# Optimization experiments

Measured on AMD Instinct MI355X. Metric: run time of the kernel, lower is better.

Reference implementation:

```python
import jax, jax.numpy as jnp
import numpy as np

D, H, E, K, N, PROJ = 512, 1024, 8, 2, 65536, 256
C = N * K // E  # expert capacity (capacity_factor=1.0 over the full token count)
LOG100 = float(np.log(100.0))


def _l2norm(v, axis=-1):
    return v / (jnp.linalg.norm(v, axis=axis, keepdims=True) + 1e-12)


def _moe(x, mask, Wp, bp, sim, temp, W1, b1, W2, b2):
    # tutel 'cosine_top' gate: cosine sim between projected tokens and expert embeddings,
    # scaled by clamped learned temperature.
    logits = _l2norm(x @ Wp + bp) @ _l2norm(sim, axis=0)
    logits = logits * jnp.exp(jnp.minimum(temp, LOG100))
    gates_all = jax.nn.softmax(logits, axis=-1)
    g, idx = jax.lax.top_k(gates_all, K)                      # [N,K]
    g = g / (jnp.sum(g, axis=-1, keepdims=True) + 1e-9)       # normalize top-k gates
    g = g * mask[:, None]                                     # zero out tokens not in this domain
    e = idx.reshape(-1)                                       # [N*K] expert id per slot
    gflat = g.reshape(-1)
    valid = jnp.repeat(mask, K)                               # [N*K]
    oh = jax.nn.one_hot(e, E, dtype=jnp.float32) * valid[:, None]
    pos = (jnp.cumsum(oh, axis=0) * oh).sum(-1).astype(jnp.int32) - 1  # slot within expert
    keep = ((pos >= 0) & (pos < C)).astype(x.dtype)           # drop overflow / masked tokens
    posc = jnp.clip(pos, 0, C - 1)
    tok = jnp.arange(N * K, dtype=jnp.int32) // K
    # dispatch -> [E,C,D]
    xd = jnp.zeros((E, C, D), x.dtype).at[e, posc].add(x[tok] * keep[:, None])
    # grouped expert FFN
    h = jax.nn.relu(jnp.einsum('ecd,edh->ech', xd, W1) + b1[:, None, :])
    y = jnp.einsum('ech,ehd->ecd', h, W2) + b2[:, None, :]
    # combine back to tokens
    out = jnp.zeros((N, D), x.dtype).at[tok].add(y[e, posc] * (gflat * keep)[:, None])
    return out


def _make_params(key):
    ks = jax.random.split(key, 4)
    Wp = jax.random.normal(ks[0], (D, PROJ), jnp.float32) * 0.02
    bp = jnp.zeros((PROJ,), jnp.float32)
    sim = jax.random.normal(ks[1], (PROJ, E), jnp.float32) * 0.02
    temp = jnp.asarray(np.log(10.0), jnp.float32)
    W1 = jax.random.normal(ks[2], (E, D, H), jnp.float32) * (1.0 / np.sqrt(D))
    b1 = jnp.zeros((E, H), jnp.float32)
    W2 = jax.random.normal(ks[3], (E, H, D), jnp.float32) * (1.0 / np.sqrt(H))
    b2 = jnp.zeros((E, D), jnp.float32)
    return Wp, bp, sim, temp, W1, b1, W2, b2


def setup_inputs():
    key = jax.random.key(0)
    kx, kl, k1, k2, k3, ksc = jax.random.split(key, 6)
    inp = {
        'x': jax.random.normal(kx, (N, D), jnp.float32),
        'domain_label': jax.random.randint(kl, (N,), 0, 2),
        'domain_scale': jax.random.normal(ksc, (1,), jnp.float32) * 0.1,
    }
    for name, k in (('sh', k1), ('day', k2), ('nt', k3)):
        Wp, bp, sim, temp, W1, b1, W2, b2 = _make_params(k)
        inp.update({name + '_Wp': Wp, name + '_bp': bp, name + '_sim': sim, name + '_temp': temp,
                    name + '_W1': W1, name + '_b1': b1, name + '_W2': W2, name + '_b2': b2})
    return inp


def reference(x, domain_label, domain_scale,
              sh_Wp, sh_bp, sh_sim, sh_temp, sh_W1, sh_b1, sh_W2, sh_b2,
              day_Wp, day_bp, day_sim, day_temp, day_W1, day_b1, day_W2, day_b2,
              nt_Wp, nt_bp, nt_sim, nt_temp, nt_W1, nt_b1, nt_W2, nt_b2):
    ones = jnp.ones((N,), jnp.float32)
    day = (domain_label == 0).astype(jnp.float32)
    night = (domain_label == 1).astype(jnp.float32)
    f_shared = _moe(x, ones, sh_Wp, sh_bp, sh_sim, sh_temp, sh_W1, sh_b1, sh_W2, sh_b2)
    f_domain = (_moe(x, day, day_Wp, day_bp, day_sim, day_temp, day_W1, day_b1, day_W2, day_b2)
                + _moe(x, night, nt_Wp, nt_bp, nt_sim, nt_temp, nt_W1, nt_b1, nt_W2, nt_b2))
    return f_shared + domain_scale * f_domain
```

## Files before the change

kernel.cpp:

```cpp
#include <hip/hip_runtime.h>

#define NTOK 65536
#define DDIM 512
#define HDIM 1024
#define NEXP 8
#define PROJ 256
#define CAP  16384
#define NSLOT (2*NTOK)
#define LOG100 4.605170185988091f

typedef __attribute__((ext_vector_type(8))) short bf16x8;
typedef __attribute__((ext_vector_type(4))) short short4v;
typedef __attribute__((ext_vector_type(4))) float f32x4;

__device__ inline float bf2f(unsigned short u){
    union { float f; unsigned int i; } c; c.i = ((unsigned int)u) << 16; return c.f;
}
__device__ inline unsigned short f2bf(float f){
    union { float f; unsigned int i; } c; c.f = f;
    unsigned int x = c.i;
    return (unsigned short)((x + 0x7fffu + ((x >> 16) & 1u)) >> 16);
}
__device__ inline void gload16(const void* g, void* lds){
    __builtin_amdgcn_global_load_lds(
        (const __attribute__((address_space(1))) unsigned int*)g,
        (__attribute__((address_space(3))) unsigned int*)lds, 16, 0, 0);
}

__global__ void init_k(const float4* __restrict__ x, ushort4* __restrict__ xb,
                       float4* __restrict__ out){
    long i = (long)blockIdx.x * 256 + threadIdx.x;
    float4 f = x[i];
    ushort4 u; u.x = f2bf(f.x); u.y = f2bf(f.y); u.z = f2bf(f.z); u.w = f2bf(f.w);
    xb[i] = u;
    out[i] = float4{0.f, 0.f, 0.f, 0.f};
}

__device__ inline void trans_body(const float* in, unsigned short* out, int R, int C){
    int rbase = blockIdx.y * 32, cbase = blockIdx.x * 32;
    if (rbase >= R || cbase >= C) return;
    __shared__ float tile[32][33];
    int tx = threadIdx.x, ty = threadIdx.y;
    #pragma unroll
    for (int i = 0; i < 4; i++)
        tile[ty + i*8][tx] = in[(long)(rbase + ty + i*8) * C + cbase + tx];
    __syncthreads();
    #pragma unroll
    for (int i = 0; i < 4; i++)
        out[(long)(cbase + ty + i*8) * R + rbase + tx] = f2bf(tile[tx][ty + i*8]);
}

__global__ __launch_bounds__(256)
void trans2_k(const float* __restrict__ W1, const float* __restrict__ W2,
              unsigned short* __restrict__ W1T, unsigned short* __restrict__ W2T)
{
    int z = blockIdx.z;
    if (z < 8) trans_body(W1 + (size_t)z*DDIM*HDIM, W1T + (size_t)z*DDIM*HDIM, DDIM, HDIM);
    else       trans_body(W2 + (size_t)(z-8)*DDIM*HDIM, W2T + (size_t)(z-8)*DDIM*HDIM, HDIM, DDIM);
}

struct W12P { const float* W1[3]; const float* W2[3]; };
__global__ __launch_bounds__(256)
void transW12all_k(W12P wp, unsigned short* __restrict__ W1T3, unsigned short* __restrict__ W2T3)
{
    int z = blockIdx.z, m = z >> 4, piece = z & 15;
    if (piece < 8)
        trans_body(wp.W1[m] + (size_t)piece*DDIM*HDIM,
                   W1T3 + ((size_t)m*8 + piece)*DDIM*HDIM, DDIM, HDIM);
    else
        trans_body(wp.W2[m] + (size_t)(piece-8)*DDIM*HDIM,
                   W2T3 + ((size_t)m*8 + piece-8)*DDIM*HDIM, HDIM, DDIM);
}

struct TpArgs { const float* Wp[3]; };
__global__ __launch_bounds__(256)
void transWp_k(TpArgs ta, unsigned short* __restrict__ WpT3)
{
    int m = blockIdx.z;
    trans_body(ta.Wp[m], WpT3 + (size_t)m*PROJ*DDIM, DDIM, PROJ);
}

struct SimArgs { const float* sim[3]; };
__global__ void simn3_k(SimArgs sa, float* __restrict__ simn3){
    __shared__ float red[256];
    const float* sim = sa.sim[blockIdx.x];
    float* simn = simn3 + (size_t)blockIdx.x * PROJ * NEXP;
    int j = threadIdx.x;
    for (int e = 0; e < NEXP; e++){
        float v = sim[j*NEXP + e];
        red[j] = v*v;
        __syncthreads();
        for (int s = 128; s > 0; s >>= 1){
            if (j < s) red[j] += red[j + s];
            __syncthreads();
        }
        float nrm = sqrtf(red[0]) + 1e-12f;
        __syncthreads();
        simn[j*NEXP + e] = v / nrm;
    }
}

struct WprodArgs { const float* Wp[3]; const float* bp[3]; };
__global__ __launch_bounds__(256)
void wprod_k(WprodArgs wa, const float* __restrict__ simn3,
             float* __restrict__ Wn3, float* __restrict__ bd3)
{
    int m = blockIdx.x;
    __shared__ float Sn[PROJ*NEXP];
    const float* Wp = wa.Wp[m];
    int t = threadIdx.x;
    for (int i = t; i < PROJ*NEXP; i += 256) Sn[i] = simn3[(size_t)m*PROJ*NEXP + i];
    __syncthreads();
    for (int r = t; r < DDIM; r += 256){
        float d[8];
        #pragma unroll
        for (int e = 0; e < 8; e++) d[e] = 0.f;
        for (int p = 0; p < PROJ; p++){
            float w = Wp[(size_t)r*PROJ + p];
            #pragma unroll
            for (int e = 0; e < 8; e++) d[e] = fmaf(w, Sn[p*8+e], d[e]);
        }
        #pragma unroll
        for (int e = 0; e < 8; e++) Wn3[((size_t)m*DDIM + r)*8 + e] = d[e];
    }
    if (t < 8){
        float s = 0.f;
        for (int p = 0; p < PROJ; p++) s = fmaf(wa.bp[m][p], Sn[p*8+t], s);
        bd3[m*8 + t] = s;
    }
}

struct PssArgs { const float* bp[3]; };
__global__ __launch_bounds__(256)
void pss_k(const unsigned short* __restrict__ WpT3, const unsigned short* __restrict__ xb,
           PssArgs pa, float* __restrict__ ssbuf)
{
    __shared__ __align__(16) short As[128*32];
    __shared__ __align__(16) short Bs[128*32];
    __shared__ float ssl[2][128];
    const int m = blockIdx.z;
    const int row0 = blockIdx.x * 128;
    const int n0 = blockIdx.y * 128;
    const unsigned short* AT = WpT3 + (size_t)m * PROJ * DDIM;
    const float* bp = pa.bp[m];

    const int t = threadIdx.x, w = t >> 6, l = t & 63;
    const int qrow = l >> 2, kc = (l & 3) * 8;
    long arowg[2], browg[2];
    #pragma unroll
    for (int q = 0; q < 2; q++){
        arowg[q] = (long)(row0 + w*32 + q*16 + qrow) * DDIM;
        browg[q] = (long)(n0   + w*32 + q*16 + qrow) * DDIM;
    }
    const int wm = (w >> 1) * 64, wn = (w & 1) * 64;
    const int fr = l & 15, fk = l >> 4;
    const int koff = fk * 8, fk4 = fk * 4;

    f32x4 acc[4][4];
    #pragma unroll
    for (int i = 0; i < 4; i++)
        #pragma unroll
        for (int j = 0; j < 4; j++) acc[i][j] = (f32x4){0.f, 0.f, 0.f, 0.f};

    for (int k0 = 0; k0 < DDIM; k0 += 32){
        __syncthreads();
        #pragma unroll
        for (int q = 0; q < 2; q++) gload16(AT + arowg[q] + k0 + kc, As + w*1024 + q*512);
        #pragma unroll
        for (int q = 0; q < 2; q++) gload16(xb + browg[q] + k0 + kc, Bs + w*1024 + q*512);
        __syncthreads();
        bf16x8 af[4], bfv[4];
        #pragma unroll
        for (int i = 0; i < 4; i++) af[i]  = *(const bf16x8*)&As[(wm + i*16 + fr)*32 + koff];
        #pragma unroll
        for (int j = 0; j < 4; j++) bfv[j] = *(const bf16x8*)&Bs[(wn + j*16 + fr)*32 + koff];
        #pragma unroll
        for (int i = 0; i < 4; i++)
            #pragma unroll
            for (int j = 0; j < 4; j++)
                acc[i][j] = __builtin_amdgcn_mfma_f32_16x16x32_bf16(af[i], bfv[j], acc[i][j], 0, 0, 0);
    }

    float part[4];
    #pragma unroll
    for (int j = 0; j < 4; j++){
        float s = 0.f;
        #pragma unroll
        for (int i = 0; i < 4; i++){
            int mc = row0 + wm + i*16 + fk4;
            float4 bb = *(const float4*)(bp + mc);
            float v0 = acc[i][j][0] + bb.x;
            float v1 = acc[i][j][1] + bb.y;
            float v2 = acc[i][j][2] + bb.z;
            float v3 = acc[i][j][3] + bb.w;
            s += v0*v0 + v1*v1 + v2*v2 + v3*v3;
        }
        s += __shfl_xor(s, 16, 64);
        s += __shfl_xor(s, 32, 64);
        part[j] = s;
    }
    if (fk == 0){
        #pragma unroll
        for (int j = 0; j < 4; j++) ssl[w >> 1][wn + j*16 + fr] = part[j];
    }
    __syncthreads();
    if (t < 128)
        ssbuf[((size_t)blockIdx.x*3 + m)*NTOK + n0 + t] = ssl[0][t] + ssl[1][t];
}

struct GfArgs { const float* tp[3]; };
__global__ __launch_bounds__(256)
void gatefin3_k(const float* __restrict__ x, const int* __restrict__ label,
                const float* __restrict__ Wn3, const float* __restrict__ bd3,
                const float* __restrict__ ssbuf, GfArgs gf,
                int* __restrict__ idx3, float* __restrict__ gw3)
{
    __shared__ float pd[3][64][26];
    const int t = threadIdx.x;
    const int tok = t & 63;
    const int qu = __builtin_amdgcn_readfirstlane(t >> 6);
    const int n = blockIdx.x * 64 + tok;

    float dots[3][8];
    #pragma unroll
    for (int m = 0; m < 3; m++)
        #pragma unroll
        for (int e = 0; e < 8; e++) dots[m][e] = 0.f;

    const float4* xp = (const float4*)(x + (size_t)n * DDIM + qu * 128);
    for (int c = 0; c < 8; c++){
        float4 xv[4];
        #pragma unroll
        for (int u = 0; u < 4; u++) xv[u] = xp[c*4 + u];
        #pragma unroll
        for (int kk = 0; kk < 16; kk++){
            float a = (kk & 2) ? ((kk & 1) ? xv[kk>>2].w : xv[kk>>2].z)
                               : ((kk & 1) ? xv[kk>>2].y : xv[kk>>2].x);
            int k = qu*128 + c*16 + kk;
            #pragma unroll
            for (int m = 0; m < 3; m++){
                const float* wr = Wn3 + ((size_t)m*DDIM + k)*8;
                float4 w0 = *(const float4*)wr;
                float4 w1 = *(const float4*)(wr + 4);
                dots[m][0] = fmaf(a, w0.x, dots[m][0]);
                dots[m][1] = fmaf(a, w0.y, dots[m][1]);
                dots[m][2] = fmaf(a, w0.z, dots[m][2]);
                dots[m][3] = fmaf(a, w0.w, dots[m][3]);
                dots[m][4] = fmaf(a, w1.x, dots[m][4]);
                dots[m][5] = fmaf(a, w1.y, dots[m][5]);
                dots[m][6] = fmaf(a, w1.z, dots[m][6]);
                dots[m][7] = fmaf(a, w1.w, dots[m][7]);
            }
        }
    }
    if (qu != 0){
        #pragma unroll
        for (int m = 0; m < 3; m++)
            #pragma unroll
            for (int e = 0; e < 8; e++) pd[qu-1][tok][m*8+e] = dots[m][e];
    }
    __syncthreads();
    if (qu == 0){
        #pragma unroll
        for (int qq = 0; qq < 3; qq++)
            #pragma unroll
            for (int m = 0; m < 3; m++)
                #pragma unroll
                for (int e = 0; e < 8; e++) dots[m][e] += pd[qq][tok][m*8+e];

        int lab = label[n];
        #pragma unroll
        for (int m = 0; m < 3; m++){
            float ss = ssbuf[(0*3+m)*(size_t)NTOK + n] + ssbuf[(1*3+m)*(size_t)NTOK + n];
            float scale = expf(fminf(gf.tp[m][0], LOG100));
            float inv = scale / (sqrtf(ss) + 1e-12f);
            float l8[8], mx = -1e30f;
            #pragma unroll
            for (int e = 0; e < 8; e++){
                l8[e] = (dots[m][e] + bd3[m*8+e]) * inv;
                mx = fmaxf(mx, l8[e]);
            }
            float g[8], s = 0.f;
            #pragma unroll
            for (int e = 0; e < 8; e++){ g[e] = expf(l8[e] - mx); s += g[e]; }
            #pragma unroll
            for (int e = 0; e < 8; e++) g[e] /= s;
            int e0 = 0; float b0 = g[0];
            #pragma unroll
            for (int e = 1; e < 8; e++) if (g[e] > b0){ b0 = g[e]; e0 = e; }
            int e1 = (e0 == 0) ? 1 : 0; float b1v = g[e1];
            #pragma unroll
            for (int e = 0; e < 8; e++) if (e != e0 && g[e] > b1v){ b1v = g[e]; e1 = e; }
            float maskv = (m == 0) ? 1.f : ((lab == m - 1) ? 1.f : 0.f);
            float s2 = b0 + b1v + 1e-9f;
            size_t base = (size_t)m * NSLOT + 2*(size_t)n;
            gw3[base]   = b0 / s2 * maskv;
            gw3[base+1] = b1v / s2 * maskv;
            idx3[base]   = e0;
            idx3[base+1] = e1;
        }
    }
}

template<int BGATHER, int OMODE>
__device__ __forceinline__
void gemm_core_t(short* As, short* Bs,
                 const unsigned short* __restrict__ AT, const unsigned short* __restrict__ Bv,
                 const float* __restrict__ bias, void* __restrict__ Cout,
                 int Kd, int Mld, int row0, int col0, int limitN,
                 const int* __restrict__ rowidx, const int* __restrict__ otok,
                 const float* __restrict__ gs)
{
    const int t = threadIdx.x;
    const int w = t >> 6, l = t & 63;
    const int qrow = l >> 2;
    const int kc = (l & 3) * 8;

    long arowg[2], browg[2];
    #pragma unroll
    for (int q = 0; q < 2; q++){
        arowg[q] = (long)(row0 + w*32 + q*16 + qrow) * Kd;
        int s = col0 + w*32 + q*16 + qrow;
        int gi = s;
        if (BGATHER) gi = (s < limitN) ? rowidx[s] : 0;
        browg[q] = (long)gi * Kd;
    }

    const int wm = (w >> 1) * 64, wn = (w & 1) * 64;
    const int fr = l & 15, fk = l >> 4;
    const int koff = fk * 8, fk4 = fk * 4;

    f32x4 acc[4][4];
    #pragma unroll
    for (int i = 0; i < 4; i++)
        #pragma unroll
        for (int j = 0; j < 4; j++) acc[i][j] = (f32x4){0.f, 0.f, 0.f, 0.f};

    for (int k0 = 0; k0 < Kd; k0 += 32){
        __syncthreads();
        #pragma unroll
        for (int q = 0; q < 2; q++) gload16(AT + arowg[q] + k0 + kc, As + w*1024 + q*512);
        #pragma unroll
        for (int q = 0; q < 2; q++) gload16(Bv + browg[q] + k0 + kc, Bs + w*1024 + q*512);
        __syncthreads();
        bf16x8 af[4], bfv[4];
        #pragma unroll
        for (int i = 0; i < 4; i++) af[i]  = *(const bf16x8*)&As[(wm + i*16 + fr)*32 + koff];
        #pragma unroll
        for (int j = 0; j < 4; j++) bfv[j] = *(const bf16x8*)&Bs[(wn + j*16 + fr)*32 + koff];
        #pragma unroll
        for (int i = 0; i < 4; i++)
            #pragma unroll
            for (int j = 0; j < 4; j++)
                acc[i][j] = __builtin_amdgcn_mfma_f32_16x16x32_bf16(af[i], bfv[j], acc[i][j], 0, 0, 0);
    }

    #pragma unroll
    for (int i = 0; i < 4; i++){
        const int mc = row0 + wm + i*16 + fk4;
        float4 bb = *(const float4*)(bias + mc);
        #pragma unroll
        for (int j = 0; j < 4; j++){
            int s = col0 + wn + j*16 + fr;
            if (s < limitN){
                if (OMODE == 1){
                    ushort4 u;
                    u.x = f2bf(fmaxf(acc[i][j][0] + bb.x, 0.f));
                    u.y = f2bf(fmaxf(acc[i][j][1] + bb.y, 0.f));
                    u.z = f2bf(fmaxf(acc[i][j][2] + bb.z, 0.f));
                    u.w = f2bf(fmaxf(acc[i][j][3] + bb.w, 0.f));
                    *(ushort4*)((unsigned short*)Cout + (long)s * Mld + mc) = u;
                } else {
                    int tk = otok[s];
                    float g = gs[s];
                    float* op = (float*)Cout + (long)tk * Mld + mc;
                    float4 c = *(const float4*)op;
                    c.x += g * (acc[i][j][0] + bb.x);
                    c.y += g * (acc[i][j][1] + bb.y);
                    c.z += g * (acc[i][j][2] + bb.z);
                    c.w += g * (acc[i][j][3] + bb.w);
                    *(float4*)op = c;
                }
            }
        }
    }
}

template<int BGATHER, int OMODE>
__device__ __forceinline__
void gemm_core_t64(short* As, short* Bs,
                   const unsigned short* __restrict__ AT, const unsigned short* __restrict__ Bv,
                   const float* __restrict__ bias, void* __restrict__ Cout,
                   int Kd, int Mld, int row0, int col0, int limitN,
                   const int* __restrict__ rowidx, const int* __restrict__ otok,
                   const float* __restrict__ gs)
{
    const int t = threadIdx.x;
    const int w = t >> 6, l = t & 63;
    const int qrow = l >> 2;
    const int seg = (l & 3) * 8;

    long arowg[2], browg[2];
    #pragma unroll
    for (int q = 0; q < 2; q++){
        arowg[q] = (long)(row0 + w*32 + q*16 + qrow) * Kd;
        int s = col0 + w*32 + q*16 + qrow;
        int gi = s;
        if (BGATHER) gi = (s < limitN) ? rowidx[s] : 0;
        browg[q] = (long)gi * Kd;
    }

    const int wm = (w >> 1) * 64, wn = (w & 1) * 64;
    const int fr = l & 15, fk = l >> 4;
    const int koff = fk * 8, fk4 = fk * 4;

    f32x4 acc[4][4];
    #pragma unroll
    for (int i = 0; i < 4; i++)
        #pragma unroll
        for (int j = 0; j < 4; j++) acc[i][j] = (f32x4){0.f, 0.f, 0.f, 0.f};

    for (int k0 = 0; k0 < Kd; k0 += 64){
        __syncthreads();
        #pragma unroll
        for (int ks = 0; ks < 2; ks++)
            #pragma unroll
            for (int q = 0; q < 2; q++)
                gload16(AT + arowg[q] + k0 + ks*32 + seg, As + ks*4096 + w*1024 + q*512);
        #pragma unroll
        for (int ks = 0; ks < 2; ks++)
            #pragma unroll
            for (int q = 0; q < 2; q++)
                gload16(Bv + browg[q] + k0 + ks*32 + seg, Bs + ks*4096 + w*1024 + q*512);
        __syncthreads();
        #pragma unroll
        for (int ks = 0; ks < 2; ks++){
            bf16x8 af[4], bfv[4];
            #pragma unroll
            for (int i = 0; i < 4; i++) af[i]  = *(const bf16x8*)&As[ks*4096 + (wm + i*16 + fr)*32 + koff];
            #pragma unroll
            for (int j = 0; j < 4; j++) bfv[j] = *(const bf16x8*)&Bs[ks*4096 + (wn + j*16 + fr)*32 + koff];
            #pragma unroll
            for (int i = 0; i < 4; i++)
                #pragma unroll
                for (int j = 0; j < 4; j++)
                    acc[i][j] = __builtin_amdgcn_mfma_f32_16x16x32_bf16(af[i], bfv[j], acc[i][j], 0, 0, 0);
        }
    }

    #pragma unroll
    for (int i = 0; i < 4; i++){
        const int mc = row0 + wm + i*16 + fk4;
        float4 bb = *(const float4*)(bias + mc);
        #pragma unroll
        for (int j = 0; j < 4; j++){
            int s = col0 + wn + j*16 + fr;
            if (s < limitN){
                if (OMODE == 1){
                    ushort4 u;
                    u.x = f2bf(fmaxf(acc[i][j][0] + bb.x, 0.f));
                    u.y = f2bf(fmaxf(acc[i][j][1] + bb.y, 0.f));
                    u.z = f2bf(fmaxf(acc[i][j][2] + bb.z, 0.f));
                    u.w = f2bf(fmaxf(acc[i][j][3] + bb.w, 0.f));
                    *(ushort4*)((unsigned short*)Cout + (long)s * Mld + mc) = u;
                } else {
                    int tk = otok[s];
                    float g = gs[s];
                    float* op = (float*)Cout + (long)tk * Mld + mc;
                    float4 c = *(const float4*)op;
                    c.x += g * (acc[i][j][0] + bb.x);
                    c.y += g * (acc[i][j][1] + bb.y);
                    c.z += g * (acc[i][j][2] + bb.z);
                    c.w += g * (acc[i][j][3] + bb.w);
                    *(float4*)op = c;
                }
            }
        }
    }
}

__device__ __forceinline__
void gemm_core_y64(short* lds,
                   const unsigned short* __restrict__ AT, const unsigned short* __restrict__ Bv,
                   const float* __restrict__ bias, float* __restrict__ out,
                   int row0, int col0, int limitN,
                   const int* __restrict__ otok, const float* __restrict__ gs)
{
    short* As = lds;
    short* Bs = lds + 4096;
    const int t = threadIdx.x, w = t >> 6, l = t & 63;
    const int seg = (l & 3) * 8;

    const long arow = (long)(row0 + w*16 + (l >> 2)) * HDIM;
    long brow[2];
    #pragma unroll
    for (int hh = 0; hh < 2; hh++)
        brow[hh] = (long)(col0 + w*32 + hh*16 + (l >> 2)) * HDIM;

    const int wm = (w >> 1) * 32, wn = (w & 1) * 64;
    const int fr = l & 15, fk = l >> 4;
    const int koff = fk * 8, fk4 = fk * 4;

    f32x4 acc[2][4];
    #pragma unroll
    for (int i = 0; i < 2; i++)
        #pragma unroll
        for (int j = 0; j < 4; j++) acc[i][j] = (f32x4){0.f, 0.f, 0.f, 0.f};

    for (int k0 = 0; k0 < HDIM; k0 += 64){
        __syncthreads();
        #pragma unroll
        for (int ks = 0; ks < 2; ks++)
            gload16(AT + arow + k0 + ks*32 + seg, As + ks*2048 + w*512);
        #pragma unroll
        for (int ks = 0; ks < 2; ks++)
            #pragma unroll
            for (int hh = 0; hh < 2; hh++)
                gload16(Bv + brow[hh] + k0 + ks*32 + seg, Bs + ks*4096 + w*1024 + hh*512);
        __syncthreads();
        #pragma unroll
        for (int ks = 0; ks < 2; ks++){
            bf16x8 af[2], bfv[4];
            #pragma unroll
            for (int i = 0; i < 2; i++)
                af[i] = *(const bf16x8*)&As[ks*2048 + (wm + i*16 + fr)*32 + koff];
            #pragma unroll
            for (int j = 0; j < 4; j++)
                bfv[j] = *(const bf16x8*)&Bs[ks*4096 + (wn + j*16 + fr)*32 + koff];
            #pragma unroll
            for (int i = 0; i < 2; i++)
                #pragma unroll
                for (int j = 0; j < 4; j++)
                    acc[i][j] = __builtin_amdgcn_mfma_f32_16x16x32_bf16(af[i], bfv[j], acc[i][j], 0, 0, 0);
        }
    }

    #pragma unroll
    for (int i = 0; i < 2; i++){
        const int mc = row0 + wm + i*16 + fk4;
        float4 bb = *(const float4*)(bias + mc);
        #pragma unroll
        for (int j = 0; j < 4; j++){
            int s = col0 + wn + j*16 + fr;
            if (s < limitN){
                int tk = otok[s];
                float g = gs[s];
                float* op = out + (long)tk * DDIM + mc;
                float4 c = *(const float4*)op;
                c.x += g * (acc[i][j][0] + bb.x);
                c.y += g * (acc[i][j][1] + bb.y);
                c.z += g * (acc[i][j][2] + bb.z);
                c.w += g * (acc[i][j][3] + bb.w);
                *(float4*)op = c;
            }
        }
    }
}

template<int BGATHER, int OMODE>
__global__ __launch_bounds__(256)
void mgemm3_k(const unsigned short* __restrict__ AT, const unsigned short* __restrict__ Bv,
              const float* __restrict__ bias, void* __restrict__ Cout,
              int Kd, int Mld,
              const int* __restrict__ rowidx, const int* __restrict__ otok,
              const float* __restrict__ gs, const int* __restrict__ cntp, int cnti)
{
    __shared__ __align__(16) short As[128*32];
    __shared__ __align__(16) short Bs[128*32];
    int limit = cntp[cnti]; if (limit > CAP) limit = CAP;
    int row0 = blockIdx.x * 128, col0 = blockIdx.y * 128;
    if (col0 >= limit) return;
    gemm_core_t<BGATHER, OMODE>(As, Bs, AT, Bv, bias, Cout, Kd, Mld,
                                row0, col0, limit, rowidx, otok, gs);
}

struct FfnP { const float* b1[3]; const float* b2[3]; };
__global__ __launch_bounds__(256)
void ffnA_k(const unsigned short* __restrict__ xb,
            const unsigned short* __restrict__ W1T3, const unsigned short* __restrict__ W2T3,
            FfnP fp, unsigned short* __restrict__ h0, unsigned short* __restrict__ h1,
            float* __restrict__ out,
            const int* __restrict__ tok3, const float* __restrict__ gslot3,
            const int* __restrict__ cntk3, int ge)
{
    __shared__ __align__(16) short lds[16384];
    const int bx = blockIdx.x, by = blockIdx.y;
    const int col0 = bx * 128;
    if (by < 8){
        if (ge >= 24) return;
        int m = ge >> 3, e = ge & 7;
        int limit = cntk3[m*16 + e]; if (limit > CAP) limit = CAP;
        if (col0 >= limit) return;
        unsigned short* hd = (ge & 1) ? h1 : h0;
        gemm_core_t64<1, 1>(lds, lds + 8192,
                            W1T3 + ((size_t)(m*8+e))*HDIM*DDIM, xb, fp.b1[m] + (size_t)e*HDIM,
                            hd, DDIM, HDIM, by*128, col0, limit,
                            tok3 + ((size_t)m*NEXP + e)*CAP, nullptr, nullptr);
    } else {
        int gy = ge - 1; if (gy < 0) return;
        int m = gy >> 3, e = gy & 7;
        int limit = cntk3[m*16 + e]; if (limit > CAP) limit = CAP;
        if (col0 >= limit) return;
        const unsigned short* hs = (gy & 1) ? h1 : h0;
        gemm_core_t64<0, 3>(lds, lds + 8192,
                            W2T3 + ((size_t)(m*8+e))*DDIM*HDIM, hs, fp.b2[m] + (size_t)e*DDIM,
                            out, HDIM, DDIM, (by-8)*128, col0, limit,
                            nullptr, tok3 + ((size_t)m*NEXP + e)*CAP,
                            gslot3 + ((size_t)m*NEXP + e)*CAP);
    }
}

__global__ __launch_bounds__(256)
void ffnB_k(const unsigned short* __restrict__ xb,
            const unsigned short* __restrict__ W1T, const float* __restrict__ b1,
            const unsigned short* __restrict__ W2T, const float* __restrict__ b2,
            unsigned short* __restrict__ h0, unsigned short* __restrict__ h1,
            float* __restrict__ out,
            const int* __restrict__ tok, const float* __restrict__ gslot,
            const int* __restrict__ cntk, int eh)
{
    __shared__ __align__(16) short lds[12288];
    const int bx = blockIdx.x, by = blockIdx.y;
    const int col0 = bx * 128;
    if (by < 8){
        if (eh > 7) return;
        int limit = cntk[eh]; if (limit > CAP) limit = CAP;
        if (col0 >= limit) return;
        unsigned short* hd = (eh & 1) ? h1 : h0;
        gemm_core_t<1, 1>(lds, lds + 4096,
                          W1T + (size_t)eh*HDIM*DDIM, xb, b1 + (size_t)eh*HDIM,
                          hd, DDIM, HDIM, by*128, col0, limit,
                          tok + (size_t)eh*CAP, nullptr, nullptr);
    } else {
        int ey = eh - 1; if (ey < 0) return;
        int limit = cntk[ey]; if (limit > CAP) limit = CAP;
        if (col0 >= limit) return;
        const unsigned short* hs = (ey & 1) ? h1 : h0;
        gemm_core_y64(lds, W2T + (size_t)ey*DDIM*HDIM, hs, b2 + (size_t)ey*DDIM,
                      out, (by-8)*64, col0, limit,
                      tok + (size_t)ey*CAP, gslot + (size_t)ey*CAP);
    }
}

__global__ __launch_bounds__(1024)
void rank_count3_k(const int* __restrict__ idx3, const int* __restrict__ label,
                   int* __restrict__ bcnt3)
{
    __shared__ int c[NEXP];
    const int m = blockIdx.y;
    const int* idx = idx3 + (size_t)m * NSLOT;
    int t = threadIdx.x;
    if (t < NEXP) c[t] = 0;
    __syncthreads();
    int s = blockIdx.x * 1024 + t;
    int n = s >> 1;
    int e = idx[s];
    bool valid = (m == 0) || (label[n] == m - 1);
    if (valid) atomicAdd(&c[e], 1);
    __syncthreads();
    if (t < NEXP) bcnt3[((size_t)m*128 + blockIdx.x)*NEXP + t] = c[t];
}

__global__ void rank_scan3_k(const int* __restrict__ bcnt3, int* __restrict__ boff3,
                             int* __restrict__ cntk3)
{
    int m = blockIdx.x, e = threadIdx.x;
    if (e < NEXP){
        int run = 0;
        for (int b = 0; b < NSLOT/1024; b++){
            boff3[((size_t)m*128 + b)*NEXP + e] = run;
            run += bcnt3[((size_t)m*128 + b)*NEXP + e];
        }
        cntk3[m*16 + e] = run < CAP ? run : CAP;
    }
}

__global__ __launch_bounds__(1024)
void rank_assign3_k(const int* __restrict__ idx3, const int* __restrict__ label,
                    const int* __restrict__ boff3, const float* __restrict__ gw3,
                    const float* __restrict__ dscale,
                    int* __restrict__ tok3, float* __restrict__ gs3)
{
    __shared__ int wcnt[16][NEXP];
    __shared__ int woff[16][NEXP];
    const int m = blockIdx.y;
    const int* idx = idx3 + (size_t)m * NSLOT;
    const float* gw = gw3 + (size_t)m * NSLOT;
    int t = threadIdx.x;
    int s = blockIdx.x * 1024 + t;
    int n = s >> 1;
    int e = idx[s];
    bool valid = (m == 0) || (label[n] == m - 1);
    int w = t >> 6, lane = t & 63;
    unsigned long long lt = (lane == 0) ? 0ull : ((1ull << lane) - 1ull);
    int myrank = 0;
    #pragma unroll
    for (int ei = 0; ei < NEXP; ei++){
        unsigned long long bal = __ballot(valid && (e == ei));
        if (ei == e) myrank = __popcll(bal & lt);
        if (lane == 0) wcnt[w][ei] = __popcll(bal);
    }
    __syncthreads();
    if (t < NEXP){
        int run = boff3[((size_t)m*128 + blockIdx.x)*NEXP + t];
        for (int w2 = 0; w2 < 16; w2++){
            woff[w2][t] = run;
            run += wcnt[w2][t];
        }
    }
    __syncthreads();
    int pos = woff[w][e] + myrank;
    bool keep = valid && (pos < CAP);
    if (keep){
        float scale = (m > 0) ? dscale[0] : 1.f;
        tok3[((size_t)m*NEXP + e)*CAP + pos] = n;
        gs3[((size_t)m*NEXP + e)*CAP + pos] = gw[s] * scale;
    }
}

extern "C" void kernel_launch(void* const* d_in, const int* in_sizes, int n_in,
                              void* d_out, int out_size, void* d_ws, size_t ws_size,
                              hipStream_t stream)
{
    (void)in_sizes; (void)n_in; (void)out_size;
    const float* x      = (const float*)d_in[0];
    const int*   label  = (const int*)  d_in[1];
    const float* dscale = (const float*)d_in[2];
    float* out = (float*)d_out;

    const size_t XB  = (size_t)NTOK * DDIM * 2;
    const size_t HS  = (size_t)CAP * HDIM * 2;
    const size_t WPT = (size_t)3 * PROJ * DDIM * 2;
    const size_t SS  = (size_t)2 * 3 * NTOK * 4;
    const size_t WN  = (size_t)3 * DDIM * 8 * 4;
    const size_t SMALL = WPT + SS + WN + 256 +
                         (size_t)3*PROJ*NEXP*4 +
                         (size_t)3*NSLOT*4*2 +
                         (size_t)3*NEXP*CAP*4*2 +
                         (size_t)3*128*NEXP*4*2 + 256;
    const size_t W12A = (size_t)2 * 3 * NEXP * DDIM * HDIM * 2;
    const size_t W12B = (size_t)2 * NEXP * DDIM * HDIM * 2;
    const size_t common = XB + HS + SMALL;

    int tier;
    if      (ws_size >= common + HS + W12A) tier = 0;
    else if (ws_size >= common + HS + W12B) tier = 1;
    else if (ws_size >= common + W12B)      tier = 2;
    else return;

    char* p = (char*)d_ws;
    unsigned short* xb   = (unsigned short*)p; p += XB;
    unsigned short* h0   = (unsigned short*)p; p += HS;
    unsigned short* WpT3 = (unsigned short*)p; p += WPT;
    float* ssbuf = (float*)p;  p += SS;
    float* Wn3   = (float*)p;  p += WN;
    float* bd3   = (float*)p;  p += 256;
    float* simn3 = (float*)p;  p += (size_t)3*PROJ*NEXP*4;
    int*   idx3  = (int*)p;    p += (size_t)3*NSLOT*4;
    float* gw3   = (float*)p;  p += (size_t)3*NSLOT*4;
    int*   tok3  = (int*)p;    p += (size_t)3*NEXP*CAP*4;
    float* gslot3= (float*)p;  p += (size_t)3*NEXP*CAP*4;
    int*   bcnt3 = (int*)p;    p += (size_t)3*128*NEXP*4;
    int*   boff3 = (int*)p;    p += (size_t)3*128*NEXP*4;
    int*   cntk3 = (int*)p;    p += 256;
    unsigned short* h1 = nullptr;
    if (tier <= 1){ h1 = (unsigned short*)p; p += HS; }
    unsigned short* Wbuf = (unsigned short*)p;

    SimArgs sa; TpArgs ta; WprodArgs wa; PssArgs pa; GfArgs gf; W12P wp; FfnP fp;
    for (int m = 0; m < 3; m++){
        ta.Wp[m] = (const float*)d_in[3 + 8*m + 0];
        wa.Wp[m] = ta.Wp[m];
        wa.bp[m] = (const float*)d_in[3 + 8*m + 1];
        pa.bp[m] = wa.bp[m];
        sa.sim[m] = (const float*)d_in[3 + 8*m + 2];
        gf.tp[m] = (const float*)d_in[3 + 8*m + 3];
        wp.W1[m] = (const float*)d_in[3 + 8*m + 4];
        fp.b1[m] = (const float*)d_in[3 + 8*m + 5];
        wp.W2[m] = (const float*)d_in[3 + 8*m + 6];
        fp.b2[m] = (const float*)d_in[3 + 8*m + 7];
    }

    init_k<<<dim3(NTOK*DDIM/4/256), dim3(256), 0, stream>>>(
        (const float4*)x, (ushort4*)xb, (float4*)out);
    simn3_k<<<dim3(3), dim3(256), 0, stream>>>(sa, simn3);
    transWp_k<<<dim3(PROJ/32, DDIM/32, 3), dim3(32,8), 0, stream>>>(ta, WpT3);
    wprod_k<<<dim3(3), dim3(256), 0, stream>>>(wa, simn3, Wn3, bd3);
    pss_k<<<dim3(2, NTOK/128, 3), dim3(256), 0, stream>>>(WpT3, xb, pa, ssbuf);
    gatefin3_k<<<dim3(NTOK/64), dim3(256), 0, stream>>>(
        x, label, Wn3, bd3, ssbuf, gf, idx3, gw3);

    rank_count3_k<<<dim3(NSLOT/1024, 3), dim3(1024), 0, stream>>>(idx3, label, bcnt3);
    rank_scan3_k<<<dim3(3), dim3(64), 0, stream>>>(bcnt3, boff3, cntk3);
    rank_assign3_k<<<dim3(NSLOT/1024, 3), dim3(1024), 0, stream>>>(
        idx3, label, boff3, gw3, dscale, tok3, gslot3);

    if (tier == 0){
        unsigned short* W1T3 = Wbuf;
        unsigned short* W2T3 = Wbuf + (size_t)3*NEXP*DDIM*HDIM;
        transW12all_k<<<dim3(32, 32, 48), dim3(32,8), 0, stream>>>(wp, W1T3, W2T3);
        for (int ge = 0; ge <= 24; ge++)
            ffnA_k<<<dim3(128, 12), 256, 0, stream>>>(
                xb, W1T3, W2T3, fp, h0, h1, out, tok3, gslot3, cntk3, ge);
    } else {
        unsigned short* W1T = Wbuf;
        unsigned short* W2T = Wbuf + (size_t)NEXP*DDIM*HDIM;
        for (int m = 0; m < 3; m++){
            trans2_k<<<dim3(32, 32, 16), dim3(32,8), 0, stream>>>(wp.W1[m], wp.W2[m], W1T, W2T);
            const int* tokm = tok3 + (size_t)m*NEXP*CAP;
            const float* gsm = gslot3 + (size_t)m*NEXP*CAP;
            const int* cntm = cntk3 + m*16;
            if (tier == 1){
                for (int eh = 0; eh <= 8; eh++)
                    ffnB_k<<<dim3(128, 16), 256, 0, stream>>>(
                        xb, W1T, fp.b1[m], W2T, fp.b2[m], h0, h1, out, tokm, gsm, cntm, eh);
            } else {
                for (int e = 0; e < NEXP; e++){
                    mgemm3_k<1, 1><<<dim3(HDIM/128, CAP/128), 256, 0, stream>>>(
                        W1T + (size_t)e*HDIM*DDIM, xb, fp.b1[m] + (size_t)e*HDIM, h0,
                        DDIM, HDIM, tokm + (size_t)e*CAP, nullptr, nullptr, cntm, e);
                    mgemm3_k<0, 3><<<dim3(DDIM/128, CAP/128), 256, 0, stream>>>(
                        W2T + (size_t)e*DDIM*HDIM, h0, fp.b2[m] + (size_t)e*DDIM, out,
                        HDIM, DDIM, nullptr, tokm + (size_t)e*CAP, gsm + (size_t)e*CAP, cntm, e);
                }
            }
        }
    }
}
```

Baseline: 1.863 ms.

## Batch day and night expert FFNs into shared launches with extra hidden buffers

Adds a new top workspace tier with two more hidden-activation buffers so the day and night MoE expert GEMMs run together in one launch per step (ffnD_k). This cuts the launch count from 25 to 17 and doubles the blocks per launch. The second GEMM also moves to a new 64-row-tile core (gemm_core_y64), which doubles its grid. In exchange it needs more workspace, and if that memory is not available it falls back to the previous path.

```diff
diff --git a/kernel.cpp b/kernel.cpp
--- a/kernel.cpp
+++ b/kernel.cpp
@@ -602,11 +602,51 @@
         int limit = cntk3[m*16 + e]; if (limit > CAP) limit = CAP;
         if (col0 >= limit) return;
         const unsigned short* hs = (gy & 1) ? h1 : h0;
-        gemm_core_t64<0, 3>(lds, lds + 8192,
-                            W2T3 + ((size_t)(m*8+e))*DDIM*HDIM, hs, fp.b2[m] + (size_t)e*DDIM,
-                            out, HDIM, DDIM, (by-8)*128, col0, limit,
-                            nullptr, tok3 + ((size_t)m*NEXP + e)*CAP,
-                            gslot3 + ((size_t)m*NEXP + e)*CAP);
+        gemm_core_y64(lds, W2T3 + ((size_t)(m*8+e))*DDIM*HDIM, hs, fp.b2[m] + (size_t)e*DDIM,
+                      out, (by-8)*64, col0, limit,
+                      tok3 + ((size_t)m*NEXP + e)*CAP, gslot3 + ((size_t)m*NEXP + e)*CAP);
+    }
+}
+
+__global__ __launch_bounds__(256)
+void ffnD_k(const unsigned short* __restrict__ xb,
+            const unsigned short* __restrict__ W1T3, const unsigned short* __restrict__ W2T3,
+            FfnP fp, unsigned short* __restrict__ h0, unsigned short* __restrict__ h1,
+            unsigned short* __restrict__ h2, unsigned short* __restrict__ h3,
+            float* __restrict__ out,
+            const int* __restrict__ tok3, const float* __restrict__ gslot3,
+            const int* __restrict__ cntk3, int s)
+{
+    __shared__ __align__(16) short lds[16384];
+    const int bx = blockIdx.x, by = blockIdx.y;
+    const int col0 = bx * 128;
+    if (by < 16){
+        if (s >= 8) return;
+        int m = (by < 8) ? 1 : 2;
+        int g = m*NEXP + s;
+        int limit = cntk3[m*16 + s]; if (limit > CAP) limit = CAP;
+        if (col0 >= limit) return;
+        unsigned short* hd = (m == 1) ? ((s & 1) ? h1 : h0) : ((s & 1) ? h3 : h2);
+        gemm_core_t64<1, 1>(lds, lds + 8192,
+                            W1T3 + (size_t)g*HDIM*DDIM, xb, fp.b1[m] + (size_t)s*HDIM,
+                            hd, DDIM, HDIM, (by & 7)*128, col0, limit,
+                            tok3 + (size_t)g*CAP, nullptr, nullptr);
+    } else {
+        int m, e; const unsigned short* hs_;
+        if (s == 0){
+            if (by >= 24) return;
+            m = 0; e = 7; hs_ = h1;
+        } else {
+            m = (by < 24) ? 1 : 2;
+            e = s - 1;
+            hs_ = (m == 1) ? ((e & 1) ? h1 : h0) : ((e & 1) ? h3 : h2);
+        }
+        int g = m*NEXP + e;
+        int limit = cntk3[m*16 + e]; if (limit > CAP) limit = CAP;
+        if (col0 >= limit) return;
+        gemm_core_y64(lds, W2T3 + (size_t)g*DDIM*HDIM, hs_, fp.b2[m] + (size_t)e*DDIM,
+                      out, ((by - 16) & 7)*64, col0, limit,
+                      tok3 + (size_t)g*CAP, gslot3 + (size_t)g*CAP);
     }
 }
 
@@ -743,9 +783,10 @@
     const size_t common = XB + HS + SMALL;
 
     int tier;
-    if      (ws_size >= common + HS + W12A) tier = 0;
-    else if (ws_size >= common + HS + W12B) tier = 1;
-    else if (ws_size >= common + W12B)      tier = 2;
+    if      (ws_size >= common + 3*HS + W12A) tier = 0;
+    else if (ws_size >= common + HS + W12A)   tier = 1;
+    else if (ws_size >= common + HS + W12B)   tier = 2;
+    else if (ws_size >= common + W12B)        tier = 3;
     else return;
 
     char* p = (char*)d_ws;
@@ -764,7 +805,10 @@
     int*   boff3 = (int*)p;    p += (size_t)3*128*NEXP*4;
     int*   cntk3 = (int*)p;    p += 256;
     unsigned short* h1 = nullptr;
-    if (tier <= 1){ h1 = (unsigned short*)p; p += HS; }
+    unsigned short* h2 = nullptr;
+    unsigned short* h3 = nullptr;
+    if (tier <= 2){ h1 = (unsigned short*)p; p += HS; }
+    if (tier == 0){ h2 = (unsigned short*)p; p += HS; h3 = (unsigned short*)p; p += HS; }
     unsigned short* Wbuf = (unsigned short*)p;
 
     SimArgs sa; TpArgs ta; WprodArgs wa; PssArgs pa; GfArgs gf; W12P wp; FfnP fp;
@@ -795,13 +839,22 @@
     rank_assign3_k<<<dim3(NSLOT/1024, 3), dim3(1024), 0, stream>>>(
         idx3, label, boff3, gw3, dscale, tok3, gslot3);
 
-    if (tier == 0){
+    if (tier <= 1){
         unsigned short* W1T3 = Wbuf;
         unsigned short* W2T3 = Wbuf + (size_t)3*NEXP*DDIM*HDIM;
         transW12all_k<<<dim3(32, 32, 48), dim3(32,8), 0, stream>>>(wp, W1T3, W2T3);
-        for (int ge = 0; ge <= 24; ge++)
-            ffnA_k<<<dim3(128, 12), 256, 0, stream>>>(
-                xb, W1T3, W2T3, fp, h0, h1, out, tok3, gslot3, cntk3, ge);
+        if (tier == 0){
+            for (int ge = 0; ge < 8; ge++)
+                ffnA_k<<<dim3(128, 16), 256, 0, stream>>>(
+                    xb, W1T3, W2T3, fp, h0, h1, out, tok3, gslot3, cntk3, ge);
+            for (int s = 0; s <= 8; s++)
+                ffnD_k<<<dim3(128, 32), 256, 0, stream>>>(
+                    xb, W1T3, W2T3, fp, h0, h1, h2, h3, out, tok3, gslot3, cntk3, s);
+        } else {
+            for (int ge = 0; ge <= 24; ge++)
+                ffnA_k<<<dim3(128, 16), 256, 0, stream>>>(
+                    xb, W1T3, W2T3, fp, h0, h1, out, tok3, gslot3, cntk3, ge);
+        }
     } else {
         unsigned short* W1T = Wbuf;
         unsigned short* W2T = Wbuf + (size_t)NEXP*DDIM*HDIM;
@@ -810,7 +863,7 @@
             const int* tokm = tok3 + (size_t)m*NEXP*CAP;
             const float* gsm = gslot3 + (size_t)m*NEXP*CAP;
             const int* cntm = cntk3 + m*16;
-            if (tier == 1){
+            if (tier == 2){
                 for (int eh = 0; eh <= 8; eh++)
                     ffnB_k<<<dim3(128, 16), 256, 0, stream>>>(
                         xb, W1T, fp.b1[m], W2T, fp.b2[m], h0, h1, out, tokm, gsm, cntm, eh);
```

Result: faster. 1.686 ms (-9.5%).
